# Optimization experiments

Measured on AMD Instinct MI355X. Metric: run time of the kernel, lower is better.

Reference implementation:

```python
import jax, jax.numpy as jnp
import numpy as np

NEG_INF = -9e15  # matches torch's -9000000000000000.0 fill for masked entries
LEAKY_SLOPE = 0.2


def setup_inputs() -> dict:
    key = jax.random.key(0)
    k1, k2, k3 = jax.random.split(key, 3)
    H, N, D = 4, 4096, 256
    x = jax.random.normal(k1, (H, N, D), dtype=jnp.float32)
    adj = jax.random.randint(k2, (N, N), 0, 2, dtype=jnp.int32)
    # per-head learned attention pattern (xavier-init dense [N,N] in the original)
    att_pattern = jax.random.normal(k3, (H, N, N), dtype=jnp.float32)
    return {"x": x, "adj": adj, "att_pattern": att_pattern,
            "is_val": 0, "epoch": 1, "layer_position": 0}


def reference(x, adj, att_pattern, is_val, epoch, layer_position):
    # x: [H, N, D], adj: [N, N], att_pattern: [H, N, N]
    # leaky_relu on the learned pattern, mask by adjacency, row softmax
    score = jax.nn.leaky_relu(att_pattern, negative_slope=LEAKY_SLOPE)
    score = jnp.where(adj[None, :, :] > 0, score, NEG_INF)
    ratio = jax.nn.softmax(score, axis=-1)  # [H, N, N]
    # dropout is identity in eval/reference mode
    out = jnp.einsum('hnm,hmd->hnd', ratio, x)  # [H, N, D]
    return out
```

## Files before the change

### kernel.cpp

```cpp
#include <hip/hip_runtime.h>

#define NHEAD 4
#define NNODE 4096
#define DIM 256
#define ROWS 32
#define CT 64
#define NT (NNODE / CT)
#define NEGV (-9e15f)

typedef float        f32x4  __attribute__((ext_vector_type(4)));
typedef int          i32x4  __attribute__((ext_vector_type(4)));
typedef unsigned int u32x2  __attribute__((ext_vector_type(2)));
typedef unsigned int u32x4  __attribute__((ext_vector_type(4)));
typedef short        bf16x8 __attribute__((ext_vector_type(8)));
typedef float        f32x16 __attribute__((ext_vector_type(16)));

__device__ __forceinline__ unsigned int f2bf(float f) {
  unsigned int u = __float_as_uint(f);
  u += 0x7fffu + ((u >> 16) & 1u);
  return u >> 16;
}

__global__ __launch_bounds__(256) void prep_all(const float* __restrict__ xg,
                                                const int* __restrict__ adj,
                                                unsigned short* __restrict__ xF,
                                                unsigned int* __restrict__ bits) {
  const int blk = blockIdx.x;
  const int t = threadIdx.x;
  if (blk < 256) {
    __shared__ unsigned short tile[64 * 260];
    const int h = blk >> 6;
    const int it = blk & 63;
    const int n = t >> 2;
    const int dsg = (t & 3) << 6;
    const float* src = xg + ((size_t)h * NNODE + (it << 6) + n) * DIM + dsg;
#pragma unroll
    for (int j = 0; j < 16; ++j) {
      const f32x4 v = *(const f32x4*)(src + 4 * j);
      u32x2 w;
      w[0] = f2bf(v[0]) | (f2bf(v[1]) << 16);
      w[1] = f2bf(v[2]) | (f2bf(v[3]) << 16);
      *(u32x2*)&tile[n * 260 + dsg + 4 * j] = w;
    }
    __syncthreads();
    const int d = t;
    unsigned short* ob = xF + ((size_t)((h << 6) + it) * 2048 + d) * 8;
#pragma unroll
    for (int ks = 0; ks < 4; ++ks)
#pragma unroll
      for (int lh = 0; lh < 2; ++lh) {
        bf16x8 val;
#pragma unroll
        for (int j = 0; j < 8; ++j) val[j] = (short)tile[(ks * 16 + lh * 8 + j) * 260 + d];
        *(bf16x8*)(ob + (size_t)(ks * 2 + lh) * 256 * 8) = val;
      }
  } else {
    const int row = blk - 256;
    const int lane = t & 63, wv = t >> 6;
#pragma unroll
    for (int rep = 0; rep < 16; ++rep) {
      const int c = (rep << 8) + t;
      const unsigned long long m = __ballot(adj[(size_t)row * NNODE + c] > 0);
      if (lane == 0) {
        bits[row * 128 + (rep << 3) + (wv << 1)]     = (unsigned int)m;
        bits[row * 128 + (rep << 3) + (wv << 1) + 1] = (unsigned int)(m >> 32);
      }
    }
  }
}

__global__ __launch_bounds__(512, 4) void gat_v4(
    const unsigned short* __restrict__ xF, const unsigned int* __restrict__ abits,
    const float* __restrict__ att, float* __restrict__ outg) {
  __shared__ unsigned short p_lds[2][ROWS * CT];
  __shared__ float l_lds[ROWS];

  const int t = threadIdx.x;
  const int lane = t & 63;
  const int flat = blockIdx.x;
  const int xcd = flat & 7;
  const int h   = xcd >> 1;
  const int rb  = ((xcd & 1) << 6) | (flat >> 3);
  const int r0  = rb * ROWS;

  const int sr  = t >> 4;
  const int c4  = (t & 15) << 2;
  const float* attb = att + ((size_t)h * NNODE + r0 + sr) * NNODE + c4;
  const unsigned int* ab = abits + (size_t)(r0 + sr) * 128 + (c4 >> 5);
  const int bsh = c4 & 31;

  const int wv   = t >> 6;
  const int d0   = wv << 5;
  const int lhi  = lane >> 5;
  const int lcol = lane & 31;
  const int axor = (lcol & 7) << 3;
  const unsigned short* xfb = xF + (size_t)h * NT * 16384 + ((lhi << 8) + d0 + lcol) * 8;

  f32x16 acc = {0.f};
  float psum = 0.f;

  bf16x8 xf0 = *(const bf16x8*)(xfb);
  bf16x8 xf1 = *(const bf16x8*)(xfb + 4096);
  bf16x8 xf2 = *(const bf16x8*)(xfb + 8192);
  bf16x8 xf3 = *(const bf16x8*)(xfb + 12288);
  f32x4 a0 = __builtin_nontemporal_load((const f32x4*)attb);
  f32x4 a1 = __builtin_nontemporal_load((const f32x4*)(attb + CT));
  f32x4 a2 = __builtin_nontemporal_load((const f32x4*)(attb + 2 * CT));
  unsigned int w0 = ab[0], w1 = ab[2], w2 = ab[4];

  int buf = 0;
  for (int it = 0; it < NT; ++it) {
    const int itn = (it + 1) & (NT - 1);
    const unsigned short* xfi = xfb + (size_t)itn * 16384;
    const bf16x8 nx0 = *(const bf16x8*)(xfi);
    const bf16x8 nx1 = *(const bf16x8*)(xfi + 4096);
    const bf16x8 nx2 = *(const bf16x8*)(xfi + 8192);
    const bf16x8 nx3 = *(const bf16x8*)(xfi + 12288);

    const int it3 = (it + 3) & (NT - 1);
    const f32x4 a3 = __builtin_nontemporal_load((const f32x4*)(attb + it3 * CT));
    const unsigned int w3 = ab[it3 << 1];

    float e0, e1, e2, e3;
    {
      float s0 = a0[0], s1 = a0[1], s2 = a0[2], s3 = a0[3];
      s0 = fmaxf(s0, 0.2f * s0); s1 = fmaxf(s1, 0.2f * s1);
      s2 = fmaxf(s2, 0.2f * s2); s3 = fmaxf(s3, 0.2f * s3);
      s0 = ((w0 >> (bsh + 0)) & 1u) ? s0 : NEGV;
      s1 = ((w0 >> (bsh + 1)) & 1u) ? s1 : NEGV;
      s2 = ((w0 >> (bsh + 2)) & 1u) ? s2 : NEGV;
      s3 = ((w0 >> (bsh + 3)) & 1u) ? s3 : NEGV;
      e0 = __expf(s0); e1 = __expf(s1); e2 = __expf(s2); e3 = __expf(s3);
      psum += (e0 + e1) + (e2 + e3);
    }
    u32x2 pk;
    pk[0] = f2bf(e0) | (f2bf(e1) << 16);
    pk[1] = f2bf(e2) | (f2bf(e3) << 16);
    *(u32x2*)&p_lds[buf][sr * CT + (c4 ^ ((sr & 7) << 3))] = pk;

    asm volatile("s_waitcnt lgkmcnt(0)" ::: "memory");
    __builtin_amdgcn_s_barrier();

    const unsigned short* pr = &p_lds[buf][lcol * CT];
    const int mkb = lhi << 3;
    const bf16x8 A0 = *(const bf16x8*)&pr[(mkb +  0) ^ axor];
    const bf16x8 A1 = *(const bf16x8*)&pr[(mkb + 16) ^ axor];
    const bf16x8 A2 = *(const bf16x8*)&pr[(mkb + 32) ^ axor];
    const bf16x8 A3 = *(const bf16x8*)&pr[(mkb + 48) ^ axor];
    acc = __builtin_amdgcn_mfma_f32_32x32x16_bf16(A0, xf0, acc, 0, 0, 0);
    acc = __builtin_amdgcn_mfma_f32_32x32x16_bf16(A1, xf1, acc, 0, 0, 0);
    acc = __builtin_amdgcn_mfma_f32_32x32x16_bf16(A2, xf2, acc, 0, 0, 0);
    acc = __builtin_amdgcn_mfma_f32_32x32x16_bf16(A3, xf3, acc, 0, 0, 0);

    a0 = a1; a1 = a2; a2 = a3;
    w0 = w1; w1 = w2; w2 = w3;
    xf0 = nx0; xf1 = nx1; xf2 = nx2; xf3 = nx3;
    buf ^= 1;
  }

  float l = psum;
  l += __shfl_xor(l, 1);
  l += __shfl_xor(l, 2);
  l += __shfl_xor(l, 4);
  l += __shfl_xor(l, 8);
  if ((t & 15) == 0) l_lds[sr] = l;
  __syncthreads();
  float* outb = outg + ((size_t)h * NNODE + r0) * DIM + d0 + lcol;
#pragma unroll
  for (int q = 0; q < 4; ++q) {
    const f32x4 lv = *(const f32x4*)&l_lds[q * 8 + lhi * 4];
    const int rbase = q * 8 + lhi * 4;
#pragma unroll
    for (int i = 0; i < 4; ++i)
      __builtin_nontemporal_store(acc[q * 4 + i] / lv[i], outb + (size_t)(rbase + i) * DIM);
  }
}

__global__ __launch_bounds__(512, 4) void gat_fused(
    const float* __restrict__ xg, const int* __restrict__ adj,
    const float* __restrict__ att, float* __restrict__ outg) {
  __shared__ __align__(16) unsigned short p_l[64 * 64];
  __shared__ __align__(16) unsigned short xT_l[DIM * 64];
  __shared__ __align__(16) float fac_l[64];
  __shared__ __align__(16) float ll_l[64];
  const int t = threadIdx.x;
  const int lane = t & 63;
  const int flat = blockIdx.x;
  const int xcd  = flat & 7;
  const int h    = xcd >> 1;
  const int rb   = ((xcd & 1) << 5) | (flat >> 3);
  const int r0   = rb * 64;
  const int srow = t >> 3;
  const int sm0  = (t & 7) << 3;
  const float* attb = att + ((size_t)h * NNODE + (r0 + srow)) * NNODE + sm0;
  const int*   adjb = adj + (size_t)(r0 + srow) * NNODE + sm0;
  const int xm0 = (t >> 5) << 2;
  const int xd0 = (t & 31) << 2;
  const float* xb_h = xg + (size_t)h * NNODE * DIM;
  const int wv   = t >> 6;
  const int d0   = wv << 5;
  const int lhi  = lane >> 5;
  const int lcol = lane & 31;
  f32x16 acc0 = {0.f};
  f32x16 acc1 = {0.f};
  float m_run = -__builtin_inff();
  float l_run = 0.f;
  for (int it = 0; it < 64; ++it) {
    const int c0 = it * 64;
    {
      const f32x4 A0 = __builtin_nontemporal_load((const f32x4*)(attb + c0));
      const f32x4 A1 = __builtin_nontemporal_load((const f32x4*)(attb + c0) + 1);
      const i32x4 j0 = *((const i32x4*)(adjb + c0));
      const i32x4 j1 = *((const i32x4*)(adjb + c0) + 1);
      float sv[8];
      int   av[8];
#pragma unroll
      for (int k = 0; k < 4; ++k) { sv[k] = A0[k]; sv[4 + k] = A1[k]; av[k] = j0[k]; av[4 + k] = j1[k]; }
#pragma unroll
      for (int k = 0; k < 8; ++k) {
        float s = sv[k];
        s = s > 0.f ? s : 0.2f * s;
        sv[k] = (av[k] > 0) ? s : NEGV;
      }
      float tmax = sv[0];
#pragma unroll
      for (int k = 1; k < 8; ++k) tmax = fmaxf(tmax, sv[k]);
      tmax = fmaxf(tmax, __shfl_xor(tmax, 1));
      tmax = fmaxf(tmax, __shfl_xor(tmax, 2));
      tmax = fmaxf(tmax, __shfl_xor(tmax, 4));
      const float m_new = fmaxf(m_run, tmax);
      float ps = 0.f;
#pragma unroll
      for (int k = 0; k < 8; ++k) { sv[k] = __expf(sv[k] - m_new); ps += sv[k]; }
      ps += __shfl_xor(ps, 1);
      ps += __shfl_xor(ps, 2);
      ps += __shfl_xor(ps, 4);
      const float fac = __expf(m_run - m_new);
      l_run = l_run * fac + ps;
      m_run = m_new;
      if ((t & 7) == 0) fac_l[srow] = fac;
      u32x4 pk;
      pk[0] = f2bf(sv[0]) | (f2bf(sv[1]) << 16);
      pk[1] = f2bf(sv[2]) | (f2bf(sv[3]) << 16);
      pk[2] = f2bf(sv[4]) | (f2bf(sv[5]) << 16);
      pk[3] = f2bf(sv[6]) | (f2bf(sv[7]) << 16);
      *(u32x4*)&p_l[srow * 64 + (sm0 ^ ((srow & 7) << 3))] = pk;
    }
    {
      const float* xb = xb_h + (size_t)(c0 + xm0) * DIM;
#pragma unroll
      for (int hh2 = 0; hh2 < 2; ++hh2) {
        const int dbase = xd0 + hh2 * 128;
        const f32x4 r0v = *(const f32x4*)(xb + dbase);
        const f32x4 r1v = *(const f32x4*)(xb + DIM + dbase);
        const f32x4 r2v = *(const f32x4*)(xb + 2 * DIM + dbase);
        const f32x4 r3v = *(const f32x4*)(xb + 3 * DIM + dbase);
#pragma unroll
        for (int j = 0; j < 4; ++j) {
          const int d = dbase + j;
          u32x2 wds;
          wds[0] = f2bf(r0v[j]) | (f2bf(r1v[j]) << 16);
          wds[1] = f2bf(r2v[j]) | (f2bf(r3v[j]) << 16);
          *(u32x2*)&xT_l[d * 64 + (xm0 ^ (((d >> 2) & 7) << 3))] = wds;
        }
      }
    }
    __syncthreads();
    {
#pragma unroll
      for (int q = 0; q < 4; ++q) {
        const f32x4 fa = *(const f32x4*)&fac_l[q * 8 + lhi * 4];
        const f32x4 fb = *(const f32x4*)&fac_l[32 + q * 8 + lhi * 4];
#pragma unroll
        for (int i = 0; i < 4; ++i) { acc0[q * 4 + i] *= fa[i]; acc1[q * 4 + i] *= fb[i]; }
      }
#pragma unroll
      for (int ks = 0; ks < 4; ++ks) {
        const int mk = ks * 16 + lhi * 8;
        const bf16x8 afA = *(const bf16x8*)&p_l[lcol * 64 + (mk ^ ((lcol & 7) << 3))];
        const bf16x8 afB = *(const bf16x8*)&p_l[(32 + lcol) * 64 + (mk ^ ((lcol & 7) << 3))];
        const int dd = d0 + lcol;
        const bf16x8 bfr = *(const bf16x8*)&xT_l[dd * 64 + (mk ^ (((dd >> 2) & 7) << 3))];
        acc0 = __builtin_amdgcn_mfma_f32_32x32x16_bf16(afA, bfr, acc0, 0, 0, 0);
        acc1 = __builtin_amdgcn_mfma_f32_32x32x16_bf16(afB, bfr, acc1, 0, 0, 0);
      }
    }
    __syncthreads();
  }
  if ((t & 7) == 0) ll_l[srow] = l_run;
  __syncthreads();
  float* outb = outg + (size_t)h * NNODE * DIM + (size_t)r0 * DIM + d0 + lcol;
#pragma unroll
  for (int q = 0; q < 4; ++q) {
    const f32x4 la = *(const f32x4*)&ll_l[q * 8 + lhi * 4];
    const f32x4 lb = *(const f32x4*)&ll_l[32 + q * 8 + lhi * 4];
    const int rbase = q * 8 + lhi * 4;
#pragma unroll
    for (int i = 0; i < 4; ++i) {
      __builtin_nontemporal_store(acc0[q * 4 + i] / la[i], outb + (size_t)(rbase + i) * DIM);
      __builtin_nontemporal_store(acc1[q * 4 + i] / lb[i], outb + (size_t)(32 + rbase + i) * DIM);
    }
  }
}

extern "C" void kernel_launch(void* const* d_in, const int* in_sizes, int n_in,
                              void* d_out, int out_size, void* d_ws, size_t ws_size,
                              hipStream_t stream) {
  const float* xg  = (const float*)d_in[0];
  const int*   adj = (const int*)d_in[1];
  const float* att = (const float*)d_in[2];
  float*       outg = (float*)d_out;
  const size_t xf_bytes = (size_t)NHEAD * DIM * NNODE * 2;
  const size_t ab_bytes = (size_t)NNODE * 128 * 4;
  if (ws_size >= xf_bytes + ab_bytes) {
    unsigned short* xF    = (unsigned short*)d_ws;
    unsigned int*   abits = (unsigned int*)((char*)d_ws + xf_bytes);
    prep_all<<<dim3(256 + NNODE), dim3(256), 0, stream>>>(xg, adj, xF, abits);
    gat_v4<<<dim3(512), dim3(512), 0, stream>>>(xF, abits, att, outg);
  } else {
    gat_fused<<<dim3(256), dim3(512), 0, stream>>>(xg, adj, att, outg);
  }
}
```

Before: 132.2 us.

## Double block size and switch to 16x16x32 MFMA tiles in main GAT kernel

The main attention kernel now runs 1024 threads per block instead of 512. Each thread handles two attention scores per tile instead of four. The MFMA work is split across 16 waves using 16x16x32 bf16 instructions on half-row/32-column subtiles, replacing 32x32x16 on 32 columns per wave. The deep software prefetch of the att and x fragments is reduced to one-tile lookahead for att only, with x loaded in the same iteration. The aim is more waves in flight to hide memory latency on the streaming att read, at the cost of lower per-thread pipelining and more barrier participants.

```diff
diff --git a/kernel.cpp b/kernel.cpp
--- a/kernel.cpp
+++ b/kernel.cpp
@@ -3,11 +3,9 @@
 #define NHEAD 4
 #define NNODE 4096
 #define DIM 256
-#define ROWS 32
-#define CT 64
-#define NT (NNODE / CT)
 #define NEGV (-9e15f)
 
+typedef float        f32x2  __attribute__((ext_vector_type(2)));
 typedef float        f32x4  __attribute__((ext_vector_type(4)));
 typedef int          i32x4  __attribute__((ext_vector_type(4)));
 typedef unsigned int u32x2  __attribute__((ext_vector_type(2)));
@@ -69,11 +67,11 @@
   }
 }
 
-__global__ __launch_bounds__(512, 4) void gat_v4(
+__global__ __launch_bounds__(1024, 8) void gat_v5(
     const unsigned short* __restrict__ xF, const unsigned int* __restrict__ abits,
     const float* __restrict__ att, float* __restrict__ outg) {
-  __shared__ unsigned short p_lds[2][ROWS * CT];
-  __shared__ float l_lds[ROWS];
+  __shared__ unsigned short p_lds[2][32 * 64];
+  __shared__ float l_lds[32];
 
   const int t = threadIdx.x;
   const int lane = t & 63;
@@ -81,81 +79,67 @@
   const int xcd = flat & 7;
   const int h   = xcd >> 1;
   const int rb  = ((xcd & 1) << 6) | (flat >> 3);
-  const int r0  = rb * ROWS;
-
-  const int sr  = t >> 4;
-  const int c4  = (t & 15) << 2;
-  const float* attb = att + ((size_t)h * NNODE + r0 + sr) * NNODE + c4;
-  const unsigned int* ab = abits + (size_t)(r0 + sr) * 128 + (c4 >> 5);
-  const int bsh = c4 & 31;
-
-  const int wv   = t >> 6;
-  const int d0   = wv << 5;
-  const int lhi  = lane >> 5;
-  const int lcol = lane & 31;
-  const int axor = (lcol & 7) << 3;
-  const unsigned short* xfb = xF + (size_t)h * NT * 16384 + ((lhi << 8) + d0 + lcol) * 8;
-
-  f32x16 acc = {0.f};
+  const int r0  = rb * 32;
+
+  const int sr = t >> 5;
+  const int c2 = (t & 31) << 1;
+  const float* attb = att + ((size_t)h * NNODE + r0 + sr) * NNODE + c2;
+  const unsigned int* ab = abits + (size_t)(r0 + sr) * 128 + (c2 >> 5);
+  const int bsh = c2 & 31;
+  const int pwoff = sr * 64 + (c2 ^ ((sr & 7) << 3));
+
+  const int wv  = t >> 6;
+  const int rh  = wv & 1;
+  const int d0  = (wv >> 1) << 5;
+  const int l15 = lane & 15;
+  const int lq  = lane >> 4;
+  const int arow = rh * 16 + l15;
+  const int akey = (arow & 7) << 3;
+  const int aoff0 = arow * 64 + ((lq * 8) ^ akey);
+  const int aoff1 = arow * 64 + ((32 + lq * 8) ^ akey);
+  const unsigned short* xfb = xF + (((size_t)h * 512 + lq) * 256 + d0 + l15) * 8;
+
+  f32x4 acc0 = {0.f, 0.f, 0.f, 0.f};
+  f32x4 acc1 = {0.f, 0.f, 0.f, 0.f};
   float psum = 0.f;
 
-  bf16x8 xf0 = *(const bf16x8*)(xfb);
-  bf16x8 xf1 = *(const bf16x8*)(xfb + 4096);
-  bf16x8 xf2 = *(const bf16x8*)(xfb + 8192);
-  bf16x8 xf3 = *(const bf16x8*)(xfb + 12288);
-  f32x4 a0 = __builtin_nontemporal_load((const f32x4*)attb);
-  f32x4 a1 = __builtin_nontemporal_load((const f32x4*)(attb + CT));
-  f32x4 a2 = __builtin_nontemporal_load((const f32x4*)(attb + 2 * CT));
-  unsigned int w0 = ab[0], w1 = ab[2], w2 = ab[4];
+  f32x2 a0 = __builtin_nontemporal_load((const f32x2*)attb);
+  unsigned int w0 = ab[0];
 
   int buf = 0;
-  for (int it = 0; it < NT; ++it) {
-    const int itn = (it + 1) & (NT - 1);
-    const unsigned short* xfi = xfb + (size_t)itn * 16384;
-    const bf16x8 nx0 = *(const bf16x8*)(xfi);
-    const bf16x8 nx1 = *(const bf16x8*)(xfi + 4096);
-    const bf16x8 nx2 = *(const bf16x8*)(xfi + 8192);
-    const bf16x8 nx3 = *(const bf16x8*)(xfi + 12288);
-
-    const int it3 = (it + 3) & (NT - 1);
-    const f32x4 a3 = __builtin_nontemporal_load((const f32x4*)(attb + it3 * CT));
-    const unsigned int w3 = ab[it3 << 1];
-
-    float e0, e1, e2, e3;
-    {
-      float s0 = a0[0], s1 = a0[1], s2 = a0[2], s3 = a0[3];
-      s0 = fmaxf(s0, 0.2f * s0); s1 = fmaxf(s1, 0.2f * s1);
-      s2 = fmaxf(s2, 0.2f * s2); s3 = fmaxf(s3, 0.2f * s3);
-      s0 = ((w0 >> (bsh + 0)) & 1u) ? s0 : NEGV;
-      s1 = ((w0 >> (bsh + 1)) & 1u) ? s1 : NEGV;
-      s2 = ((w0 >> (bsh + 2)) & 1u) ? s2 : NEGV;
-      s3 = ((w0 >> (bsh + 3)) & 1u) ? s3 : NEGV;
-      e0 = __expf(s0); e1 = __expf(s1); e2 = __expf(s2); e3 = __expf(s3);
-      psum += (e0 + e1) + (e2 + e3);
-    }
-    u32x2 pk;
-    pk[0] = f2bf(e0) | (f2bf(e1) << 16);
-    pk[1] = f2bf(e2) | (f2bf(e3) << 16);
-    *(u32x2*)&p_lds[buf][sr * CT + (c4 ^ ((sr & 7) << 3))] = pk;
+  for (int it = 0; it < 64; ++it) {
+    const int it1 = (it + 1) & 63;
+    const f32x2 an = __builtin_nontemporal_load((const f32x2*)(attb + it1 * 64));
+    const unsigned int wn = ab[it1 << 1];
+
+    const unsigned short* xfi = xfb + (size_t)it * 16384;
+    const bf16x8 B00 = *(const bf16x8*)(xfi);
+    const bf16x8 B01 = *(const bf16x8*)(xfi + 128);
+    const bf16x8 B10 = *(const bf16x8*)(xfi + 8192);
+    const bf16x8 B11 = *(const bf16x8*)(xfi + 8320);
+
+    float s0 = a0[0], s1 = a0[1];
+    s0 = fmaxf(s0, 0.2f * s0);
+    s1 = fmaxf(s1, 0.2f * s1);
+    s0 = ((w0 >> bsh) & 1u) ? s0 : NEGV;
+    s1 = ((w0 >> (bsh + 1)) & 1u) ? s1 : NEGV;
+    const float e0 = __expf(s0), e1 = __expf(s1);
+    psum += e0 + e1;
+    const unsigned int pk = f2bf(e0) | (f2bf(e1) << 16);
+    *(unsigned int*)&p_lds[buf][pwoff] = pk;
 
     asm volatile("s_waitcnt lgkmcnt(0)" ::: "memory");
     __builtin_amdgcn_s_barrier();
 
-    const unsigned short* pr = &p_lds[buf][lcol * CT];
-    const int mkb = lhi << 3;
-    const bf16x8 A0 = *(const bf16x8*)&pr[(mkb +  0) ^ axor];
-    const bf16x8 A1 = *(const bf16x8*)&pr[(mkb + 16) ^ axor];
-    const bf16x8 A2 = *(const bf16x8*)&pr[(mkb + 32) ^ axor];
-    const bf16x8 A3 = *(const bf16x8*)&pr[(mkb + 48) ^ axor];
-    acc = __builtin_amdgcn_mfma_f32_32x32x16_bf16(A0, xf0, acc, 0, 0, 0);
-    acc = __builtin_amdgcn_mfma_f32_32x32x16_bf16(A1, xf1, acc, 0, 0, 0);
-    acc = __builtin_amdgcn_mfma_f32_32x32x16_bf16(A2, xf2, acc, 0, 0, 0);
-    acc = __builtin_amdgcn_mfma_f32_32x32x16_bf16(A3, xf3, acc, 0, 0, 0);
-
-    a0 = a1; a1 = a2; a2 = a3;
-    w0 = w1; w1 = w2; w2 = w3;
-    xf0 = nx0; xf1 = nx1; xf2 = nx2; xf3 = nx3;
-    buf ^= 1;
+    const unsigned short* pb = p_lds[buf];
+    const bf16x8 A0 = *(const bf16x8*)&pb[aoff0];
+    const bf16x8 A1 = *(const bf16x8*)&pb[aoff1];
+    acc0 = __builtin_amdgcn_mfma_f32_16x16x32_bf16(A0, B00, acc0, 0, 0, 0);
+    acc1 = __builtin_amdgcn_mfma_f32_16x16x32_bf16(A0, B01, acc1, 0, 0, 0);
+    acc0 = __builtin_amdgcn_mfma_f32_16x16x32_bf16(A1, B10, acc0, 0, 0, 0);
+    acc1 = __builtin_amdgcn_mfma_f32_16x16x32_bf16(A1, B11, acc1, 0, 0, 0);
+
+    a0 = an; w0 = wn; buf ^= 1;
   }
 
   float l = psum;
@@ -163,16 +147,15 @@
   l += __shfl_xor(l, 2);
   l += __shfl_xor(l, 4);
   l += __shfl_xor(l, 8);
-  if ((t & 15) == 0) l_lds[sr] = l;
+  l += __shfl_xor(l, 16);
+  if ((lane & 31) == 0) l_lds[sr] = l;
   __syncthreads();
-  float* outb = outg + ((size_t)h * NNODE + r0) * DIM + d0 + lcol;
-#pragma unroll
-  for (int q = 0; q < 4; ++q) {
-    const f32x4 lv = *(const f32x4*)&l_lds[q * 8 + lhi * 4];
-    const int rbase = q * 8 + lhi * 4;
-#pragma unroll
-    for (int i = 0; i < 4; ++i)
-      __builtin_nontemporal_store(acc[q * 4 + i] / lv[i], outb + (size_t)(rbase + i) * DIM);
+  const f32x4 lv = *(const f32x4*)&l_lds[rh * 16 + lq * 4];
+  float* outb = outg + ((size_t)h * NNODE + r0 + rh * 16 + lq * 4) * DIM + d0 + l15;
+#pragma unroll
+  for (int i = 0; i < 4; ++i) {
+    __builtin_nontemporal_store(acc0[i] / lv[i], outb + (size_t)i * DIM);
+    __builtin_nontemporal_store(acc1[i] / lv[i], outb + (size_t)i * DIM + 16);
   }
 }
 
@@ -316,7 +299,7 @@
     unsigned short* xF    = (unsigned short*)d_ws;
     unsigned int*   abits = (unsigned int*)((char*)d_ws + xf_bytes);
     prep_all<<<dim3(256 + NNODE), dim3(256), 0, stream>>>(xg, adj, xF, abits);
-    gat_v4<<<dim3(512), dim3(512), 0, stream>>>(xF, abits, att, outg);
+    gat_v5<<<dim3(512), dim3(1024), 0, stream>>>(xF, abits, att, outg);
   } else {
     gat_fused<<<dim3(256), dim3(512), 0, stream>>>(xg, adj, att, outg);
   }
```

Result: slower. 148.4 us (+12.2%).
